# Kernel optimization log

Measured on AMD Instinct MI355X. Metric: run time of the kernel, lower is better.

## Reference

```python
import jax, jax.numpy as jnp
import numpy as np

EMB = 512
NUM_HEAD = 8
HEAD_DIM = EMB // NUM_HEAD  # 64
B, S = 16, 2048


def setup_inputs() -> dict:
    key = jax.random.key(0)
    k1, k2, k3, k4 = jax.random.split(key, 4)
    x1 = jax.random.normal(k1, (B, S, EMB), dtype=jnp.float32)
    # causal mask: 1 where attention allowed, 0 elsewhere (masked_fill where mask==0)
    mask = jnp.tril(jnp.ones((S, S), dtype=jnp.int32))
    scale = 1.0 / np.sqrt(EMB)
    Wq = jax.random.normal(k2, (EMB, HEAD_DIM), dtype=jnp.float32) * scale
    Wk = jax.random.normal(k3, (EMB, HEAD_DIM), dtype=jnp.float32) * scale
    Wv = jax.random.normal(k4, (EMB, HEAD_DIM), dtype=jnp.float32) * scale
    return {"x1": x1, "mask": mask, "Wq": Wq, "Wk": Wk, "Wv": Wv}


def reference(x1, mask, Wq, Wk, Wv):
    # q,k,v: [B,S,H]
    q = jnp.einsum('bse,eh->bsh', x1, Wq)
    k = jnp.einsum('bse,eh->bsh', x1, Wk)
    v = jnp.einsum('bse,eh->bsh', x1, Wv)
    # scores: [B,S,S]
    scaled_qk = jnp.einsum('bqh,bkh->bqk', q, k) / jnp.sqrt(jnp.float32(HEAD_DIM))
    scaled_qk = jnp.where(mask == 0, -jnp.inf, scaled_qk)
    attn = jax.nn.softmax(scaled_qk, axis=-1)
    return jnp.einsum('bqk,bkh->bqh', attn, v)
```

## Files before the change

### kernel.cpp

```cpp
#include <hip/hip_runtime.h>
#include <hip/hip_bf16.h>

typedef __attribute__((ext_vector_type(8))) short bf16x8;
typedef __attribute__((ext_vector_type(4))) float f32x4;
typedef __attribute__((ext_vector_type(4))) unsigned short u16x4;

#define MFMA16(a, b, c) __builtin_amdgcn_mfma_f32_16x16x32_bf16(a, b, c, 0, 0, 0)

#define QSCALE 0.18033688011112042f

#define GLDS16(gp, lp)                                                         \
    __builtin_amdgcn_global_load_lds(                                          \
        (const __attribute__((address_space(1))) void*)(gp),                   \
        (__attribute__((address_space(3))) void*)(lp), 16, 0, 0)

__device__ __forceinline__ short nbf(float f) {
    __hip_bfloat16 h = __float2bfloat16(f);
    return *(short*)&h;
}
__device__ __forceinline__ unsigned short nbfu(float f) {
    __hip_bfloat16 h = __float2bfloat16(f);
    return *(unsigned short*)&h;
}

__global__ void wt_kernel(const float* __restrict__ Wq, const float* __restrict__ Wk,
                          const float* __restrict__ Wv, unsigned short* __restrict__ Wt) {
    const int h = blockIdx.x;
    const int mat = blockIdx.y;
    const int e = threadIdx.x;
    const float* W = (mat == 0) ? Wq : ((mat == 1) ? Wk : Wv);
    Wt[(mat * 64 + h) * 512 + e] = nbfu(W[e * 64 + h]);
}

__global__ __launch_bounds__(512, 1) void qkv_proj(
    const float* __restrict__ x1, const unsigned short* __restrict__ Wt,
    unsigned short* __restrict__ Q, unsigned short* __restrict__ K,
    unsigned short* __restrict__ Vt)
{
    __shared__ char alds[2][16384];
    __shared__ char blds[2][12288];

    const int tid = threadIdx.x;
    const int W = tid >> 6, lane = tid & 63;
    const int c = lane & 15, g = lane >> 4;
    const int tokB = blockIdx.x * 128;

    const char* x1b = (const char*)x1;
    const char* Wtb = (const char*)Wt;

    const int tA0 = tid >> 3,           qA0 = (tid & 7) ^ (tA0 & 7);
    const int tA1 = (tid + 512) >> 3,   qA1 = (tid & 7) ^ (tA1 & 7);
    const size_t aoff0 = (size_t)(tokB + tA0) * 2048 + qA0 * 16;
    const size_t aoff1 = (size_t)(tokB + tA1) * 2048 + qA1 * 16;

    auto bsrc = [&](int j) -> size_t {
        const int n = j >> 6, c2 = (j >> 2) & 15, g2 = j & 3;
        return (size_t)((n >> 2) * 64 + (n & 3) * 16 + c2) * 1024 + g2 * 16;
    };
    const size_t boff0 = bsrc(tid), boff1 = bsrc(tid + 512);

    f32x4 acc[12];
#pragma unroll
    for (int n = 0; n < 12; ++n) acc[n] = (f32x4)0.f;

    GLDS16(x1b + aoff0, &alds[0][tid * 16]);
    GLDS16(x1b + aoff1, &alds[0][8192 + tid * 16]);
    GLDS16(Wtb + boff0, &blds[0][tid * 16]);
    if (tid < 256) GLDS16(Wtb + boff1, &blds[0][8192 + tid * 16]);

    const int arow = (W * 16 + c) * 128;
    const int aq0 = (((2 * g) ^ (c & 7)) * 16);
    const int aq1 = (((2 * g + 1) ^ (c & 7)) * 16);
    const int brd = (c * 4 + g) * 16;

    int buf = 0;
    for (int ks = 0; ks < 16; ++ks) {
        asm volatile("s_waitcnt vmcnt(0)\n\ts_barrier" ::: "memory");

        if (ks < 15) {
            const size_t ka = (size_t)(ks + 1) * 128;
            const size_t kb = (size_t)(ks + 1) * 64;
            char* ab = &alds[buf ^ 1][0];
            char* bb = &blds[buf ^ 1][0];
            GLDS16(x1b + aoff0 + ka, ab + tid * 16);
            GLDS16(x1b + aoff1 + ka, ab + 8192 + tid * 16);
            GLDS16(Wtb + boff0 + kb, bb + tid * 16);
            if (tid < 256) GLDS16(Wtb + boff1 + kb, bb + 8192 + tid * 16);
        }

        const char* ab = &alds[buf][0];
        const char* bb = &blds[buf][0];
        f32x4 a0 = *(const f32x4*)(ab + arow + aq0);
        f32x4 a1 = *(const f32x4*)(ab + arow + aq1);
        bf16x8 af;
        af[0] = nbf(a0[0]); af[1] = nbf(a0[1]); af[2] = nbf(a0[2]); af[3] = nbf(a0[3]);
        af[4] = nbf(a1[0]); af[5] = nbf(a1[1]); af[6] = nbf(a1[2]); af[7] = nbf(a1[3]);
#pragma unroll
        for (int n = 0; n < 12; ++n) {
            bf16x8 bf = *(const bf16x8*)(bb + n * 1024 + brd);
            acc[n] = MFMA16(af, bf, acc[n]);
        }
        buf ^= 1;
    }

    const int tok0 = tokB + W * 16;
#pragma unroll
    for (int n = 0; n < 4; ++n)
#pragma unroll
        for (int r = 0; r < 4; ++r)
            Q[(size_t)(tok0 + g * 4 + r) * 64 + n * 16 + c] = nbfu(acc[n][r] * QSCALE);
#pragma unroll
    for (int n = 0; n < 4; ++n)
#pragma unroll
        for (int r = 0; r < 4; ++r)
            K[(size_t)(tok0 + g * 4 + r) * 64 + n * 16 + c] = nbfu(acc[4 + n][r]);

    const int b = tok0 >> 11;
    const int sl = (tok0 & 2047) + g * 4;
#pragma unroll
    for (int n = 0; n < 4; ++n) {
        const int d = n * 16 + c;
        u16x4 pv;
#pragma unroll
        for (int r = 0; r < 4; ++r) pv[r] = nbfu(acc[8 + n][r]);
        *(u16x4*)(Vt + ((size_t)(b * 64 + d) << 11) + sl) = pv;
    }
}

__global__ __launch_bounds__(512, 1) void flash_attn(
    const unsigned short* __restrict__ Q, const unsigned short* __restrict__ K,
    const unsigned short* __restrict__ Vt, float* __restrict__ out)
{
    __shared__ char kv[2][65536];
    __shared__ char p_lds[32768];

    const int tid = threadIdx.x;
    const int W = tid >> 6;
    const int st = W >> 2;
    const int w = W & 3;
    const int lane = tid & 63;
    const int c = lane & 15, g = lane >> 4;

    const int id = blockIdx.x;
    const int b = 2 * (id & 7) + ((id >> 3) & 1);
    const int qt = 31 - (id >> 4);
    const int n2 = (qt >> 1) + 1;
    const int J = (n2 + 1) >> 1;
    const int qr0c = qt * 64 + w * 16 + c;
    const size_t qrow_g = ((size_t)b << 11) + qt * 64 + w * 16;

    bf16x8 qf0 = *(const bf16x8*)(Q + (qrow_g + c) * 64 + g * 8);
    bf16x8 qf1 = *(const bf16x8*)(Q + (qrow_g + c) * 64 + 32 + g * 8);

    const char* Kb = (const char*)(K + (((size_t)b << 11) * 64));
    const char* Vb = (const char*)(Vt + (((size_t)b << 11) * 64));

    const int c2 = tid & 15, g2 = (tid >> 4) & 3, nn = (tid >> 6) & 3, s4 = (tid >> 8) & 1;
    const int koff = (nn * 16 + c2) * 128 + g2 * 16 + s4 * 64;
    const int voff = (nn * 16 + c2) * 4096 + g2 * 16 + s4 * 64;

    float m = -1e30f, l = 0.f;
    f32x4 acc[4];
#pragma unroll
    for (int n = 0; n < 4; ++n) acc[n] = (f32x4)0.f;

    {
        char* d = &kv[0][0];
        GLDS16(Kb + koff,                 d + tid * 16);
        GLDS16(Kb + koff + 8192,          d + 8192 + tid * 16);
        GLDS16(Vb + voff,                 d + 16384 + tid * 16);
        GLDS16(Vb + voff + 128,           d + 16384 + 8192 + tid * 16);
        GLDS16(Kb + 16384 + koff,         d + 32768 + tid * 16);
        GLDS16(Kb + 16384 + koff + 8192,  d + 32768 + 8192 + tid * 16);
        GLDS16(Vb + 256 + voff,           d + 49152 + tid * 16);
        GLDS16(Vb + 256 + voff + 128,     d + 49152 + 8192 + tid * 16);
    }

    for (int j = 0; j < J; ++j) {
        asm volatile("s_waitcnt vmcnt(0)\n\ts_barrier" ::: "memory");

        if (j + 1 < J) {
            const size_t kA = (size_t)(2 * j + 2) * 16384;
            const size_t vA = (size_t)(2 * j + 2) * 256;
            char* d = &kv[(j & 1) ^ 1][0];
            GLDS16(Kb + kA + koff,                 d + tid * 16);
            GLDS16(Kb + kA + koff + 8192,          d + 8192 + tid * 16);
            GLDS16(Vb + vA + voff,                 d + 16384 + tid * 16);
            GLDS16(Vb + vA + voff + 128,           d + 16384 + 8192 + tid * 16);
            GLDS16(Kb + kA + 16384 + koff,         d + 32768 + tid * 16);
            GLDS16(Kb + kA + 16384 + koff + 8192,  d + 32768 + 8192 + tid * 16);
            GLDS16(Vb + vA + 256 + voff,           d + 49152 + tid * 16);
            GLDS16(Vb + vA + 256 + voff + 128,     d + 49152 + 8192 + tid * 16);
        }

        const int t = 2 * j + st;
        if (t < n2) {
            const char* kb = &kv[j & 1][st * 32768];
            const char* vb = kb + 16384;

            f32x4 s[8];
#pragma unroll
            for (int i = 0; i < 8; ++i) s[i] = (f32x4)0.f;
            __builtin_amdgcn_s_setprio(1);
#pragma unroll
            for (int h = 0; h < 2; ++h)
#pragma unroll
                for (int n = 0; n < 4; ++n) {
                    bf16x8 ka0 = *(const bf16x8*)(kb + h * 8192 + n * 1024 + lane * 16);
                    bf16x8 ka1 = *(const bf16x8*)(kb + h * 8192 + 4096 + n * 1024 + lane * 16);
                    s[h * 4 + n] = MFMA16(ka0, qf0, s[h * 4 + n]);
                    s[h * 4 + n] = MFMA16(ka1, qf1, s[h * 4 + n]);
                }
            __builtin_amdgcn_s_setprio(0);

            if (t == n2 - 1) {
#pragma unroll
                for (int h = 0; h < 2; ++h)
#pragma unroll
                    for (int n = 0; n < 4; ++n) {
                        const int key0 = t * 128 + h * 64 + n * 16 + g * 4;
#pragma unroll
                        for (int r = 0; r < 4; ++r)
                            if (key0 + r > qr0c) s[h * 4 + n][r] = -1e30f;
                    }
            }

            float tm = -1e30f;
#pragma unroll
            for (int i = 0; i < 8; ++i)
                tm = fmaxf(tm, fmaxf(fmaxf(s[i][0], s[i][1]), fmaxf(s[i][2], s[i][3])));

            if (__any(tm > m + 8.f)) {
                float gm = tm;
                gm = fmaxf(gm, __shfl_xor(gm, 16, 64));
                gm = fmaxf(gm, __shfl_xor(gm, 32, 64));
                const float mn = fmaxf(m, gm);
                const float alpha = exp2f(m - mn);
                m = mn;
                l *= alpha;
                float al[4];
#pragma unroll
                for (int r = 0; r < 4; ++r) al[r] = __shfl(alpha, g * 4 + r, 16);
#pragma unroll
                for (int n = 0; n < 4; ++n)
#pragma unroll
                    for (int r = 0; r < 4; ++r) acc[n][r] *= al[r];
            }

            char* pw = &p_lds[W * 4096 + ((g >> 1) * 16 + c) * 16 + (g & 1) * 8];
#pragma unroll
            for (int h = 0; h < 2; ++h)
#pragma unroll
                for (int n = 0; n < 4; ++n) {
                    const int i = h * 4 + n;
                    float p0 = exp2f(s[i][0] - m);
                    float p1 = exp2f(s[i][1] - m);
                    float p2 = exp2f(s[i][2] - m);
                    float p3 = exp2f(s[i][3] - m);
                    l += (p0 + p1) + (p2 + p3);
                    u16x4 pk;
                    pk[0] = nbfu(p0); pk[1] = nbfu(p1); pk[2] = nbfu(p2); pk[3] = nbfu(p3);
                    *(u16x4*)(pw + (h * 2 + (n >> 1)) * 1024 + (n & 1) * 512) = pk;
                }

            const char* pr = &p_lds[W * 4096 + lane * 16];
            bf16x8 pf[4];
#pragma unroll
            for (int ps = 0; ps < 4; ++ps) pf[ps] = *(const bf16x8*)(pr + ps * 1024);
            __builtin_amdgcn_s_setprio(1);
#pragma unroll
            for (int n = 0; n < 4; ++n) {
#pragma unroll
                for (int ps = 0; ps < 4; ++ps) {
                    bf16x8 vf = *(const bf16x8*)(vb + (ps >> 1) * 8192 + (ps & 1) * 4096 + n * 1024 + lane * 16);
                    acc[n] = MFMA16(pf[ps], vf, acc[n]);
                }
            }
            __builtin_amdgcn_s_setprio(0);
        }
    }

    __syncthreads();
    float* accb = (float*)&kv[0][0];
    float* mb = (float*)&kv[0][16384];
    float* lb = (float*)&kv[0][16384 + 256];

    if (st == 1) {
        l += __shfl_xor(l, 16, 64);
        l += __shfl_xor(l, 32, 64);
        if (g == 0) { mb[w * 16 + c] = m; lb[w * 16 + c] = l; }
#pragma unroll
        for (int n = 0; n < 4; ++n)
#pragma unroll
            for (int r = 0; r < 4; ++r)
                accb[w * 1024 + (g * 4 + r) * 64 + n * 16 + c] = acc[n][r];
    }
    __syncthreads();

    if (st == 0) {
        l += __shfl_xor(l, 16, 64);
        l += __shfl_xor(l, 32, 64);
        const float m1c = mb[w * 16 + c];
        const float l1c = lb[w * 16 + c];
        const float mF = fmaxf(m, m1c);
        const float a0 = exp2f(m - mF);
        const float a1 = (m1c > -1e29f) ? exp2f(m1c - mF) : 0.f;
        const float inv = 1.f / (l * a0 + l1c * a1);
        const float s0 = a0 * inv, s1 = a1 * inv;
        float s0r[4], s1r[4];
#pragma unroll
        for (int r = 0; r < 4; ++r) {
            s0r[r] = __shfl(s0, g * 4 + r, 16);
            s1r[r] = __shfl(s1, g * 4 + r, 16);
        }
#pragma unroll
        for (int n = 0; n < 4; ++n)
#pragma unroll
            for (int r = 0; r < 4; ++r) {
                const float a1v = accb[w * 1024 + (g * 4 + r) * 64 + n * 16 + c];
                out[(qrow_g + g * 4 + r) * 64 + n * 16 + c] = acc[n][r] * s0r[r] + a1v * s1r[r];
            }
    }
}

extern "C" void kernel_launch(void* const* d_in, const int* in_sizes, int n_in,
                              void* d_out, int out_size, void* d_ws, size_t ws_size,
                              hipStream_t stream) {
    const float* x1 = (const float*)d_in[0];
    const float* Wq = (const float*)d_in[2];
    const float* Wk = (const float*)d_in[3];
    const float* Wv = (const float*)d_in[4];
    float* out = (float*)d_out;

    unsigned short* Wt  = (unsigned short*)d_ws;
    unsigned short* Qw  = (unsigned short*)((char*)d_ws + 196608);
    unsigned short* Kw  = (unsigned short*)((char*)d_ws + 196608 + 4194304);
    unsigned short* Vtw = (unsigned short*)((char*)d_ws + 196608 + 2 * 4194304);

    wt_kernel<<<dim3(64, 3), 512, 0, stream>>>(Wq, Wk, Wv, Wt);
    qkv_proj<<<256, 512, 0, stream>>>(x1, Wt, Qw, Kw, Vtw);
    flash_attn<<<512, 512, 0, stream>>>(Qw, Kw, Vtw, out);
}
```

Measured before the change: 65.24 us.

## Pre-swizzle K and V into fragment-ordered tiles for contiguous LDS staging

The projection kernel now writes K and V straight into a per-64-token-tile layout that matches the MFMA fragment order. This lets the attention kernel stage each tile with fully contiguous 16-byte global-to-LDS copies instead of strided, transposed addressing. The attention kernel also preloads all K fragments into registers before the QK MFMAs. Its launch bound is raised to 2 blocks per CU, although its 160KB of shared memory likely still limits occupancy to one. The extra K registers add register pressure.

```diff
diff --git a/kernel.cpp b/kernel.cpp
--- a/kernel.cpp
+++ b/kernel.cpp
@@ -34,8 +34,8 @@
 
 __global__ __launch_bounds__(512, 1) void qkv_proj(
     const float* __restrict__ x1, const unsigned short* __restrict__ Wt,
-    unsigned short* __restrict__ Q, unsigned short* __restrict__ K,
-    unsigned short* __restrict__ Vt)
+    unsigned short* __restrict__ Q, unsigned short* __restrict__ Kf,
+    unsigned short* __restrict__ Vf)
 {
     __shared__ char alds[2][16384];
     __shared__ char blds[2][12288];
@@ -104,32 +104,45 @@
     }
 
     const int tok0 = tokB + W * 16;
+    const int bb2 = tokB >> 11;
+    const int ht = ((tokB & 2047) >> 6) + (W >> 2);
+
 #pragma unroll
     for (int n = 0; n < 4; ++n)
 #pragma unroll
         for (int r = 0; r < 4; ++r)
             Q[(size_t)(tok0 + g * 4 + r) * 64 + n * 16 + c] = nbfu(acc[n][r] * QSCALE);
-#pragma unroll
-    for (int n = 0; n < 4; ++n)
-#pragma unroll
-        for (int r = 0; r < 4; ++r)
-            K[(size_t)(tok0 + g * 4 + r) * 64 + n * 16 + c] = nbfu(acc[4 + n][r]);
-
-    const int b = tok0 >> 11;
-    const int sl = (tok0 & 2047) + g * 4;
-#pragma unroll
-    for (int n = 0; n < 4; ++n) {
-        const int d = n * 16 + c;
-        u16x4 pv;
-#pragma unroll
-        for (int r = 0; r < 4; ++r) pv[r] = nbfu(acc[8 + n][r]);
-        *(u16x4*)(Vt + ((size_t)(b * 64 + d) << 11) + sl) = pv;
-    }
-}
-
-__global__ __launch_bounds__(512, 1) void flash_attn(
-    const unsigned short* __restrict__ Q, const unsigned short* __restrict__ K,
-    const unsigned short* __restrict__ Vt, float* __restrict__ out)
+
+    {
+        unsigned short* kf = Kf + (size_t)bb2 * 131072 + (size_t)ht * 4096;
+#pragma unroll
+        for (int n = 0; n < 4; ++n) {
+            const int gf = (n & 1) * 2 + (c >> 3);
+            const size_t base = (size_t)(n >> 1) * 2048 + (W & 3) * 512 + (c & 7);
+#pragma unroll
+            for (int r = 0; r < 4; ++r)
+                kf[base + (size_t)(gf * 16 + g * 4 + r) * 8] = nbfu(acc[4 + n][r]);
+        }
+    }
+
+    {
+        unsigned short* vf = Vf + (size_t)bb2 * 131072 + (size_t)ht * 4096;
+        const int sub = (W & 3) >> 1;
+        const int gf = (W & 1) * 2 + (g >> 1);
+        const int jb = (g & 1) * 4;
+#pragma unroll
+        for (int n = 0; n < 4; ++n) {
+            u16x4 pv;
+#pragma unroll
+            for (int r = 0; r < 4; ++r) pv[r] = nbfu(acc[8 + n][r]);
+            *(u16x4*)(vf + (size_t)sub * 2048 + n * 512 + (gf * 16 + c) * 8 + jb) = pv;
+        }
+    }
+}
+
+__global__ __launch_bounds__(512, 2) void flash_attn(
+    const unsigned short* __restrict__ Q, const unsigned short* __restrict__ Kf,
+    const unsigned short* __restrict__ Vf, float* __restrict__ out)
 {
     __shared__ char kv[2][65536];
     __shared__ char p_lds[32768];
@@ -152,65 +165,58 @@
     bf16x8 qf0 = *(const bf16x8*)(Q + (qrow_g + c) * 64 + g * 8);
     bf16x8 qf1 = *(const bf16x8*)(Q + (qrow_g + c) * 64 + 32 + g * 8);
 
-    const char* Kb = (const char*)(K + (((size_t)b << 11) * 64));
-    const char* Vb = (const char*)(Vt + (((size_t)b << 11) * 64));
-
-    const int c2 = tid & 15, g2 = (tid >> 4) & 3, nn = (tid >> 6) & 3, s4 = (tid >> 8) & 1;
-    const int koff = (nn * 16 + c2) * 128 + g2 * 16 + s4 * 64;
-    const int voff = (nn * 16 + c2) * 4096 + g2 * 16 + s4 * 64;
+    const char* Kfb = (const char*)(Kf + (size_t)b * 131072);
+    const char* Vfb = (const char*)(Vf + (size_t)b * 131072);
+
+    const int off0 = tid * 16, off1 = (tid + 512) * 16;
 
     float m = -1e30f, l = 0.f;
     f32x4 acc[4];
 #pragma unroll
     for (int n = 0; n < 4; ++n) acc[n] = (f32x4)0.f;
 
-    {
-        char* d = &kv[0][0];
-        GLDS16(Kb + koff,                 d + tid * 16);
-        GLDS16(Kb + koff + 8192,          d + 8192 + tid * 16);
-        GLDS16(Vb + voff,                 d + 16384 + tid * 16);
-        GLDS16(Vb + voff + 128,           d + 16384 + 8192 + tid * 16);
-        GLDS16(Kb + 16384 + koff,         d + 32768 + tid * 16);
-        GLDS16(Kb + 16384 + koff + 8192,  d + 32768 + 8192 + tid * 16);
-        GLDS16(Vb + 256 + voff,           d + 49152 + tid * 16);
-        GLDS16(Vb + 256 + voff + 128,     d + 49152 + 8192 + tid * 16);
-    }
+    auto STAGE = [&](int p, char* d) {
+        const size_t o0 = (size_t)(2 * p) * 16384;
+        const size_t o1 = o0 + 16384;
+        GLDS16(Kfb + o0 + off0, d + off0);
+        GLDS16(Kfb + o0 + off1, d + off1);
+        GLDS16(Vfb + o0 + off0, d + 16384 + off0);
+        GLDS16(Vfb + o0 + off1, d + 16384 + off1);
+        GLDS16(Kfb + o1 + off0, d + 32768 + off0);
+        GLDS16(Kfb + o1 + off1, d + 32768 + off1);
+        GLDS16(Vfb + o1 + off0, d + 49152 + off0);
+        GLDS16(Vfb + o1 + off1, d + 49152 + off1);
+    };
+
+    STAGE(0, &kv[0][0]);
 
     for (int j = 0; j < J; ++j) {
         asm volatile("s_waitcnt vmcnt(0)\n\ts_barrier" ::: "memory");
 
-        if (j + 1 < J) {
-            const size_t kA = (size_t)(2 * j + 2) * 16384;
-            const size_t vA = (size_t)(2 * j + 2) * 256;
-            char* d = &kv[(j & 1) ^ 1][0];
-            GLDS16(Kb + kA + koff,                 d + tid * 16);
-            GLDS16(Kb + kA + koff + 8192,          d + 8192 + tid * 16);
-            GLDS16(Vb + vA + voff,                 d + 16384 + tid * 16);
-            GLDS16(Vb + vA + voff + 128,           d + 16384 + 8192 + tid * 16);
-            GLDS16(Kb + kA + 16384 + koff,         d + 32768 + tid * 16);
-            GLDS16(Kb + kA + 16384 + koff + 8192,  d + 32768 + 8192 + tid * 16);
-            GLDS16(Vb + vA + 256 + voff,           d + 49152 + tid * 16);
-            GLDS16(Vb + vA + 256 + voff + 128,     d + 49152 + 8192 + tid * 16);
-        }
+        if (j + 1 < J) STAGE(j + 1, &kv[(j & 1) ^ 1][0]);
 
         const int t = 2 * j + st;
         if (t < n2) {
             const char* kb = &kv[j & 1][st * 32768];
             const char* vb = kb + 16384;
 
+            bf16x8 kfA[8], kfB[8];
+#pragma unroll
+            for (int h = 0; h < 2; ++h)
+#pragma unroll
+                for (int n = 0; n < 4; ++n) {
+                    kfA[h * 4 + n] = *(const bf16x8*)(kb + h * 8192 + n * 1024 + lane * 16);
+                    kfB[h * 4 + n] = *(const bf16x8*)(kb + h * 8192 + 4096 + n * 1024 + lane * 16);
+                }
             f32x4 s[8];
 #pragma unroll
             for (int i = 0; i < 8; ++i) s[i] = (f32x4)0.f;
             __builtin_amdgcn_s_setprio(1);
 #pragma unroll
-            for (int h = 0; h < 2; ++h)
-#pragma unroll
-                for (int n = 0; n < 4; ++n) {
-                    bf16x8 ka0 = *(const bf16x8*)(kb + h * 8192 + n * 1024 + lane * 16);
-                    bf16x8 ka1 = *(const bf16x8*)(kb + h * 8192 + 4096 + n * 1024 + lane * 16);
-                    s[h * 4 + n] = MFMA16(ka0, qf0, s[h * 4 + n]);
-                    s[h * 4 + n] = MFMA16(ka1, qf1, s[h * 4 + n]);
-                }
+            for (int i = 0; i < 8; ++i) {
+                s[i] = MFMA16(kfA[i], qf0, s[i]);
+                s[i] = MFMA16(kfB[i], qf1, s[i]);
+            }
             __builtin_amdgcn_s_setprio(0);
 
             if (t == n2 - 1) {
@@ -267,15 +273,15 @@
             bf16x8 pf[4];
 #pragma unroll
             for (int ps = 0; ps < 4; ++ps) pf[ps] = *(const bf16x8*)(pr + ps * 1024);
+
             __builtin_amdgcn_s_setprio(1);
 #pragma unroll
-            for (int n = 0; n < 4; ++n) {
+            for (int n = 0; n < 4; ++n)
 #pragma unroll
                 for (int ps = 0; ps < 4; ++ps) {
                     bf16x8 vf = *(const bf16x8*)(vb + (ps >> 1) * 8192 + (ps & 1) * 4096 + n * 1024 + lane * 16);
                     acc[n] = MFMA16(pf[ps], vf, acc[n]);
                 }
-            }
             __builtin_amdgcn_s_setprio(0);
         }
     }
@@ -334,10 +340,10 @@
 
     unsigned short* Wt  = (unsigned short*)d_ws;
     unsigned short* Qw  = (unsigned short*)((char*)d_ws + 196608);
-    unsigned short* Kw  = (unsigned short*)((char*)d_ws + 196608 + 4194304);
-    unsigned short* Vtw = (unsigned short*)((char*)d_ws + 196608 + 2 * 4194304);
+    unsigned short* Kfw = (unsigned short*)((char*)d_ws + 196608 + 4194304);
+    unsigned short* Vfw = (unsigned short*)((char*)d_ws + 196608 + 2 * 4194304);
 
     wt_kernel<<<dim3(64, 3), 512, 0, stream>>>(Wq, Wk, Wv, Wt);
-    qkv_proj<<<256, 512, 0, stream>>>(x1, Wt, Qw, Kw, Vtw);
-    flash_attn<<<512, 512, 0, stream>>>(Qw, Kw, Vtw, out);
-}
+    qkv_proj<<<256, 512, 0, stream>>>(x1, Wt, Qw, Kfw, Vfw);
+    flash_attn<<<512, 512, 0, stream>>>(Qw, Kfw, Vfw, out);
+}
```

Result: faster. 57.93 us (-11.2%).
